# Performance work log

Hardware: AMD Instinct MI355X
Metric: run time of the kernel (lower is better)

The kernel has to match this reference:

```python
import jax, jax.numpy as jnp
import numpy as np


def setup_inputs() -> dict:
    key = jax.random.key(0)
    ks = jax.random.split(key, 5)
    B, S, D = 2, 2048, 1024
    inv = 1.0 / np.sqrt(D)
    inp = {
        "x": jax.random.normal(ks[0], (B, S, D), jnp.float32),
        "Wq": jax.random.normal(ks[1], (D, D), jnp.float32) * inv,
        "bq": jnp.zeros((D,), jnp.float32),
        "Wk": jax.random.normal(ks[2], (D, D), jnp.float32) * inv,
        "bk": jnp.zeros((D,), jnp.float32),
        "Wv": jax.random.normal(ks[3], (D, D), jnp.float32) * inv,
        "bv": jnp.zeros((D,), jnp.float32),
        "Wo": jax.random.normal(ks[4], (D, D), jnp.float32) * inv,
        "bo": jnp.zeros((D,), jnp.float32),
        "num_heads": 16,
        "window_size": 128,
    }
    return inp


def reference(x, Wq, bq, Wk, bk, Wv, bv, Wo, bo, num_heads, window_size):
    B, S, D = x.shape
    H = num_heads
    hd = D // H
    scale = 1.0 / np.sqrt(hd)

    def split_heads(t):  # [B,S,D] -> [B,H,S,hd]
        return t.reshape(B, S, H, hd).transpose(0, 2, 1, 3)

    q = split_heads(x @ Wq + bq)
    k = split_heads(x @ Wk + bk)
    v = split_heads(x @ Wv + bv)

    # dense scores, then sliding-window + causal mask (faithful to original)
    scores = jnp.einsum('bhqd,bhkd->bhqk', q, k) * scale  # [B,H,S,S]
    i = jnp.arange(S)[:, None]
    j = jnp.arange(S)[None, :]
    # position i attends to j in [i - window_size + 1, i]
    mask = (j <= i) & (j > i - window_size)
    scores = jnp.where(mask, scores, -jnp.inf)
    attn_weights = jax.nn.softmax(scores, axis=-1)  # dropout is identity in eval

    out = jnp.einsum('bhqk,bhkd->bhqd', attn_weights, v)  # [B,H,S,hd]
    out = out.transpose(0, 2, 1, 3).reshape(B, S, D)
    return out @ Wo + bo, attn_weights
```

## Files before the change

kernel.cpp:

```cpp
#include <hip/hip_runtime.h>
#include <cmath>

typedef __attribute__((ext_vector_type(8))) __bf16 v8bf;
typedef __attribute__((ext_vector_type(4))) float  v4f;

#define DEV static __device__ __forceinline__

DEV unsigned short f2bf(float f) {
  unsigned u = __builtin_bit_cast(unsigned, f);
  unsigned r = u + 0x7fffu + ((u >> 16) & 1u);
  return (unsigned short)(r >> 16);
}
DEV float bf2f(unsigned short s) {
  return __builtin_bit_cast(float, ((unsigned)s) << 16);
}
DEV v8bf ld8(const unsigned short* p) { return *(const v8bf*)p; }

DEV void gl16(const unsigned short* g, unsigned short* l) {
  __builtin_amdgcn_global_load_lds(
      (const __attribute__((address_space(1))) unsigned int*)g,
      (__attribute__((address_space(3))) unsigned int*)l, 16, 0, 0);
}

DEV void zero_rows(float* __restrict__ wout, int rbase, int wave, int lane) {
  int r0 = rbase + wave * 4;
  for (int rr = 0; rr < 4; rr++) {
    int row = r0 + rr;
    int i = row & 2047;
    int lo = i - 127;
    float* rowp = wout + (size_t)row * 2048;
#pragma unroll
    for (int it = 0; it < 8; it++) {
      int col = it * 256 + lane * 4;
      bool full_in = (col >= lo) && (col + 3 <= i);
      if (full_in) continue;
      bool overlap = (col + 3 >= lo) && (col <= i);
      if (!overlap) {
        v4f z = {0.f, 0.f, 0.f, 0.f};
        __builtin_nontemporal_store(z, (v4f*)(rowp + col));
      } else {
#pragma unroll
        for (int e = 0; e < 4; e++) {
          int j = col + e;
          if (j < lo || j > i) rowp[j] = 0.f;
        }
      }
    }
  }
}

__global__ __launch_bounds__(256) void k_prep(const float* __restrict__ x,
                                              const float* __restrict__ Wq,
                                              const float* __restrict__ Wk,
                                              const float* __restrict__ Wv,
                                              const float* __restrict__ Wo,
                                              const float* __restrict__ bq,
                                              const float* __restrict__ bk,
                                              const float* __restrict__ bv,
                                              unsigned short* __restrict__ xb,
                                              unsigned short* __restrict__ WT,
                                              unsigned short* __restrict__ WoT,
                                              float* __restrict__ bqkv) {
  __shared__ float t[32][33];
  int bx = blockIdx.x, tid = threadIdx.x;
  if (bx < 4096) {
    int i = bx * 256 + tid;
    float4 v = ((const float4*)x)[i];
    unsigned lo = (unsigned)f2bf(v.x) | ((unsigned)f2bf(v.y) << 16);
    unsigned hi = (unsigned)f2bf(v.z) | ((unsigned)f2bf(v.w) << 16);
    ((uint2*)xb)[i] = make_uint2(lo, hi);
  } else if (bx < 8192) {
    int rem = bx - 4096;
    int z = rem >> 10, r2 = rem & 1023;
    const float* src = (z == 0) ? Wq : (z == 1) ? Wk : (z == 2) ? Wv : Wo;
    unsigned short* dst = (z < 3) ? WT + z * 1048576 : WoT;
    int n0 = (r2 & 31) * 32, k0 = (r2 >> 5) * 32;
    int tx = tid & 31, ty = tid >> 5;
    for (int r = ty; r < 32; r += 8)
      t[r][tx] = src[(k0 + r) * 1024 + n0 + tx];
    __syncthreads();
    for (int r = ty; r < 32; r += 8)
      dst[(n0 + r) * 1024 + k0 + tx] = f2bf(t[tx][r]);
  } else {
    int i = (bx - 8192) * 256 + tid;
    float v = (i < 1024) ? bq[i] : (i < 2048 ? bk[i - 1024] : bv[i - 2048]);
    bqkv[i] = v;
  }
}

__global__ __launch_bounds__(256) void k_gemm1(const unsigned short* __restrict__ A,
                                               const unsigned short* __restrict__ Bt,
                                               const float* __restrict__ bias,
                                               unsigned short* __restrict__ Cout,
                                               float* __restrict__ wout) {
  constexpr int K = 1024;
  __shared__ __attribute__((aligned(16))) unsigned short As[128 * 32];
  __shared__ __attribute__((aligned(16))) unsigned short Bs[128 * 32];
  int tid = threadIdx.x;
  int wave = tid >> 6, lane = tid & 63;
  int bx = blockIdx.x;
  if (!(bx % 3 == 0 && bx < 2304)) {
    int wid = (bx < 2304) ? (bx - (bx + 2) / 3) : (1536 + bx - 2304);
    zero_rows(wout, wid * 16, wave, lane);
    return;
  }
  int gid = bx / 3;
  int n0 = (gid % 24) * 128, m0 = (gid / 24) * 128;
  int wm = (wave >> 1) * 64, wn = (wave & 1) * 64;
  int m = lane & 15, q4 = lane >> 4;
  int arow = tid >> 2, acol = (tid & 3) * 8;
  v4f acc[4][4] = {};
  const unsigned short* ga0 = A + (m0 + arow) * K + acol;
  const unsigned short* ga1 = A + (m0 + 64 + arow) * K + acol;
  const unsigned short* gb0 = Bt + (n0 + arow) * K + acol;
  const unsigned short* gb1 = Bt + (n0 + 64 + arow) * K + acol;
  unsigned short* lA0 = As + wave * 512;
  unsigned short* lA1 = As + 2048 + wave * 512;
  unsigned short* lB0 = Bs + wave * 512;
  unsigned short* lB1 = Bs + 2048 + wave * 512;

  for (int kt = 0; kt < K; kt += 32) {
    gl16(ga0 + kt, lA0);
    gl16(ga1 + kt, lA1);
    gl16(gb0 + kt, lB0);
    gl16(gb1 + kt, lB1);
    __syncthreads();
    v8bf af[4], bfv[4];
#pragma unroll
    for (int mt = 0; mt < 4; mt++) af[mt] = ld8(&As[(wm + mt * 16 + m) * 32 + q4 * 8]);
#pragma unroll
    for (int nt = 0; nt < 4; nt++) bfv[nt] = ld8(&Bs[(wn + nt * 16 + m) * 32 + q4 * 8]);
#pragma unroll
    for (int mt = 0; mt < 4; mt++)
#pragma unroll
      for (int nt = 0; nt < 4; nt++)
        acc[mt][nt] = __builtin_amdgcn_mfma_f32_16x16x32_bf16(af[mt], bfv[nt], acc[mt][nt], 0, 0, 0);
    __syncthreads();
  }
#pragma unroll
  for (int mt = 0; mt < 4; mt++)
#pragma unroll
    for (int nt = 0; nt < 4; nt++) {
      int col = n0 + wn + nt * 16 + m;
      float bb = bias[col];
#pragma unroll
      for (int r = 0; r < 4; r++) {
        int row = m0 + wm + mt * 16 + q4 * 4 + r;
        Cout[row * 3072 + col] = f2bf(acc[mt][nt][r] + bb);
      }
    }
}

__global__ __launch_bounds__(256) void k_transv(const unsigned short* __restrict__ QKV,
                                                unsigned short* __restrict__ Vtg) {
  __shared__ unsigned short t[32][33];
  int bx = blockIdx.x, tid = threadIdx.x;
  int st = bx & 63, h2 = (bx >> 6) & 1, bh = bx >> 7;
  int b = bh >> 4, h = bh & 15;
  int s0 = st * 32, d0 = h2 * 32;
  int tx = tid & 31, ty = tid >> 5;
  const unsigned short* src = QKV + (size_t)b * 2048 * 3072 + 2048 + h * 64 + d0;
  for (int r = ty; r < 32; r += 8)
    t[r][tx] = src[(size_t)(s0 + r) * 3072 + tx];
  __syncthreads();
  unsigned short* dst = Vtg + (size_t)(bh * 64 + d0) * 2048 + s0;
  for (int r = ty; r < 32; r += 8)
    dst[(size_t)r * 2048 + tx] = t[tx][r];
}

__global__ __launch_bounds__(256) void k_attn(const unsigned short* __restrict__ QKV,
                                              const unsigned short* __restrict__ Vtg,
                                              unsigned short* __restrict__ Oatt,
                                              float* __restrict__ wout) {
  constexpr int VTS = 208;
  constexpr int PSS = 168;
  __shared__ __attribute__((aligned(16))) unsigned short Vt[64 * VTS];
  __shared__ __attribute__((aligned(16))) unsigned short Ps[4][16 * PSS];
  int tid = threadIdx.x, wave = tid >> 6, lane = tid & 63;
  int bx = blockIdx.x;
  if (bx >= 32) {
    int wid = (bx - 32) + 40 * (blockIdx.y + 16 * blockIdx.z);
    zero_rows(wout, 28672 + wid * 16, wave, lane);
    return;
  }
  int b = blockIdx.z, h = blockIdx.y, i0 = bx * 64;
  int kbase = i0 - 128;
  const int ld = 3072;
  const unsigned short* Qg = QKV + b * 2048 * ld + h * 64;
  const unsigned short* Kg = Qg + 1024;

  const unsigned short* vsrc = Vtg + (size_t)(b * 16 + h) * 64 * 2048;
  for (int idx = tid; idx < 1536; idx += 256) {
    int row = idx / 24, c16 = idx % 24;
    int gcol = kbase + c16 * 8;
    if (gcol < 0) gcol = 0;
    v8bf vv = ld8(vsrc + (size_t)row * 2048 + gcol);
    *(v8bf*)&Vt[row * VTS + c16 * 8] = vv;
  }
  {
    int row = tid >> 2, c4 = (tid & 3) * 4;
    *(uint2*)&Vt[row * VTS + 192 + c4] = make_uint2(0u, 0u);
  }
  for (int c = lane; c < 16 * 24; c += 64)
    Ps[wave][(c / 24) * PSS + 144 + (c % 24)] = 0;
  __syncthreads();

  int qb = i0 + wave * 16;
  int m = lane & 15, q4 = lane >> 4;

  const unsigned short* qrow = Qg + (qb + m) * ld;
  v8bf qa0 = ld8(qrow + q4 * 8);
  v8bf qa1 = ld8(qrow + 32 + q4 * 8);

  v4f sc[9];
#pragma unroll
  for (int n = 0; n < 9; n++) {
    int key = kbase + wave * 16 + n * 16 + m;
    int kg = key < 0 ? 0 : key;
    const unsigned short* krow = Kg + kg * ld;
    v8bf kb0 = ld8(krow + q4 * 8);
    v8bf kb1 = ld8(krow + 32 + q4 * 8);
    v4f z = {0.f, 0.f, 0.f, 0.f};
    z = __builtin_amdgcn_mfma_f32_16x16x32_bf16(qa0, kb0, z, 0, 0, 0);
    z = __builtin_amdgcn_mfma_f32_16x16x32_bf16(qa1, kb1, z, 0, 0, 0);
    sc[n] = z;
  }
  float mx[4] = {-3e38f, -3e38f, -3e38f, -3e38f};
#pragma unroll
  for (int n = 0; n < 9; n++)
#pragma unroll
    for (int r = 0; r < 4; r++) {
      int i = qb + q4 * 4 + r;
      int j = kbase + wave * 16 + n * 16 + m;
      float v = sc[n][r] * 0.125f;
      bool ok = (j >= 0) && (j <= i) && (j > i - 128);
      v = ok ? v : -3e38f;
      sc[n][r] = v;
      mx[r] = fmaxf(mx[r], v);
    }
#pragma unroll
  for (int o = 1; o < 16; o <<= 1)
#pragma unroll
    for (int r = 0; r < 4; r++) mx[r] = fmaxf(mx[r], __shfl_xor(mx[r], o, 64));
  float sum[4] = {0.f, 0.f, 0.f, 0.f};
#pragma unroll
  for (int n = 0; n < 9; n++)
#pragma unroll
    for (int r = 0; r < 4; r++) {
      float p = __expf(sc[n][r] - mx[r]);
      sc[n][r] = p;
      sum[r] += p;
    }
#pragma unroll
  for (int o = 1; o < 16; o <<= 1)
#pragma unroll
    for (int r = 0; r < 4; r++) sum[r] += __shfl_xor(sum[r], o, 64);
  float inv[4];
#pragma unroll
  for (int r = 0; r < 4; r++) inv[r] = 1.0f / sum[r];

#pragma unroll
  for (int n = 0; n < 9; n++)
#pragma unroll
    for (int r = 0; r < 4; r++)
      Ps[wave][(q4 * 4 + r) * PSS + n * 16 + m] = f2bf(sc[n][r] * inv[r]);
  __syncthreads();

  v4f oacc[4] = {};
#pragma unroll
  for (int c = 0; c < 5; c++) {
    v8bf pa = ld8(&Ps[wave][m * PSS + c * 32 + q4 * 8]);
#pragma unroll
    for (int dt = 0; dt < 4; dt++) {
      v8bf vb = ld8(&Vt[(dt * 16 + m) * VTS + wave * 16 + c * 32 + q4 * 8]);
      oacc[dt] = __builtin_amdgcn_mfma_f32_16x16x32_bf16(pa, vb, oacc[dt], 0, 0, 0);
    }
  }
#pragma unroll
  for (int dt = 0; dt < 4; dt++)
#pragma unroll
    for (int r = 0; r < 4; r++)
      Oatt[(b * 2048 + qb + q4 * 4 + r) * 1024 + h * 64 + dt * 16 + m] = f2bf(oacc[dt][r]);

  for (int R = 0; R < 16; R++) {
    int iq = qb + R;
    float* rowp = wout + (size_t)((b * 16 + h) * 2048 + iq) * 2048;
    int lo = iq - 127;
    int t0 = R + 1 + lane * 2;
    float p0 = bf2f(Ps[wave][R * PSS + t0]);
    float p1 = bf2f(Ps[wave][R * PSS + t0 + 1]);
    int j0 = lo + lane * 2;
    if (j0 >= 0) rowp[j0] = p0;
    if (j0 + 1 >= 0) rowp[j0 + 1] = p1;
  }
}

__global__ __launch_bounds__(256) void k_tail(const unsigned short* __restrict__ Oat,
                                              const unsigned short* __restrict__ WoT,
                                              const float* __restrict__ bo,
                                              float* __restrict__ out,
                                              float* __restrict__ wout) {
  __shared__ __attribute__((aligned(16))) unsigned short As[128 * 32];
  __shared__ __attribute__((aligned(16))) unsigned short Bs[128 * 32];
  int tid = threadIdx.x, wave = tid >> 6, lane = tid & 63;
  int bx = blockIdx.x;

  if (bx % 5 != 0) {
    int wid = bx - (bx + 4) / 5;
    zero_rows(wout, 49152 + wid * 16, wave, lane);
    return;
  }
  constexpr int K = 1024;
  int gid = bx / 5;
  int n0 = (gid & 7) * 128, m0 = (gid >> 3) * 128;
  int wm = (wave >> 1) * 64, wn = (wave & 1) * 64;
  int m = lane & 15, q4 = lane >> 4;
  int arow = tid >> 2, acol = (tid & 3) * 8;
  v4f acc[4][4] = {};
  const unsigned short* ga0 = Oat + (m0 + arow) * K + acol;
  const unsigned short* ga1 = Oat + (m0 + 64 + arow) * K + acol;
  const unsigned short* gb0 = WoT + (n0 + arow) * K + acol;
  const unsigned short* gb1 = WoT + (n0 + 64 + arow) * K + acol;
  unsigned short* lA0 = As + wave * 512;
  unsigned short* lA1 = As + 2048 + wave * 512;
  unsigned short* lB0 = Bs + wave * 512;
  unsigned short* lB1 = Bs + 2048 + wave * 512;
  for (int kt = 0; kt < K; kt += 32) {
    gl16(ga0 + kt, lA0);
    gl16(ga1 + kt, lA1);
    gl16(gb0 + kt, lB0);
    gl16(gb1 + kt, lB1);
    __syncthreads();
    v8bf af[4], bfv[4];
#pragma unroll
    for (int mt = 0; mt < 4; mt++) af[mt] = ld8(&As[(wm + mt * 16 + m) * 32 + q4 * 8]);
#pragma unroll
    for (int nt = 0; nt < 4; nt++) bfv[nt] = ld8(&Bs[(wn + nt * 16 + m) * 32 + q4 * 8]);
#pragma unroll
    for (int mt = 0; mt < 4; mt++)
#pragma unroll
      for (int nt = 0; nt < 4; nt++)
        acc[mt][nt] = __builtin_amdgcn_mfma_f32_16x16x32_bf16(af[mt], bfv[nt], acc[mt][nt], 0, 0, 0);
    __syncthreads();
  }
#pragma unroll
  for (int mt = 0; mt < 4; mt++)
#pragma unroll
    for (int nt = 0; nt < 4; nt++) {
      int col = n0 + wn + nt * 16 + m;
      float bb = bo[col];
#pragma unroll
      for (int r = 0; r < 4; r++) {
        int row = m0 + wm + mt * 16 + q4 * 4 + r;
        out[row * 1024 + col] = acc[mt][nt][r] + bb;
      }
    }
}

extern "C" void kernel_launch(void* const* d_in, const int* in_sizes, int n_in,
                              void* d_out, int out_size, void* d_ws, size_t ws_size,
                              hipStream_t stream) {
  (void)in_sizes; (void)n_in; (void)out_size; (void)ws_size;
  const float* x  = (const float*)d_in[0];
  const float* Wq = (const float*)d_in[1];
  const float* bq = (const float*)d_in[2];
  const float* Wk = (const float*)d_in[3];
  const float* bk = (const float*)d_in[4];
  const float* Wv = (const float*)d_in[5];
  const float* bv = (const float*)d_in[6];
  const float* Wo = (const float*)d_in[7];
  const float* bo = (const float*)d_in[8];

  char* ws = (char*)d_ws;
  unsigned short* xb   = (unsigned short*)(ws);
  unsigned short* WT   = (unsigned short*)(ws + 8388608);
  unsigned short* WoT  = (unsigned short*)(ws + 14680064);
  float*          bqkv = (float*)(ws + 16777216);
  unsigned short* QKV  = (unsigned short*)(ws + 16789504);
  unsigned short* Oat  = (unsigned short*)(ws + 41955328);
  unsigned short* Vtg  = (unsigned short*)(ws + 67121152);

  float* out  = (float*)d_out;
  float* wout = out + 4194304;

  k_prep<<<8204, 256, 0, stream>>>(x, Wq, Wk, Wv, Wo, bq, bk, bv, xb, WT, WoT, bqkv);
  k_gemm1<<<2560, 256, 0, stream>>>(xb, WT, bqkv, QKV, wout);
  k_transv<<<4096, 256, 0, stream>>>(QKV, Vtg);
  k_attn<<<dim3(72, 16, 2), 256, 0, stream>>>(QKV, Vtg, Oat, wout);
  k_tail<<<1280, 256, 0, stream>>>(Oat, WoT, bo, out, wout);
}
```

Measured before the change: 653.4 us.

## Fuse V transpose into QKV GEMM epilogue and interleave weight zeroing

The QKV GEMM epilogue now writes Q and K into a compact buffer and writes V directly in transposed per-head layout, which removes the separate transpose kernel and its round trip through memory. The zero-fill of the large attention-weights output is redistributed. Each GEMM block issues non-temporal zero stores inside its K loop instead of using separate zeroing blocks, attention blocks zero extra rows after their main work, and the tail kernel takes the remainder. This lets the streaming writes overlap with compute, at the cost of extra store traffic competing with GEMM loads and an uncoalesced 8-byte strided write pattern for V.

```diff
diff --git a/kernel.cpp b/kernel.cpp
--- a/kernel.cpp
+++ b/kernel.cpp
@@ -91,20 +91,15 @@
 __global__ __launch_bounds__(256) void k_gemm1(const unsigned short* __restrict__ A,
                                                const unsigned short* __restrict__ Bt,
                                                const float* __restrict__ bias,
-                                               unsigned short* __restrict__ Cout,
+                                               unsigned short* __restrict__ QK,
+                                               unsigned short* __restrict__ Vtg,
                                                float* __restrict__ wout) {
   constexpr int K = 1024;
   __shared__ __attribute__((aligned(16))) unsigned short As[128 * 32];
   __shared__ __attribute__((aligned(16))) unsigned short Bs[128 * 32];
   int tid = threadIdx.x;
   int wave = tid >> 6, lane = tid & 63;
-  int bx = blockIdx.x;
-  if (!(bx % 3 == 0 && bx < 2304)) {
-    int wid = (bx < 2304) ? (bx - (bx + 2) / 3) : (1536 + bx - 2304);
-    zero_rows(wout, wid * 16, wave, lane);
-    return;
-  }
-  int gid = bx / 3;
+  int gid = blockIdx.x;
   int n0 = (gid % 24) * 128, m0 = (gid / 24) * 128;
   int wm = (wave >> 1) * 64, wn = (wave & 1) * 64;
   int m = lane & 15, q4 = lane >> 4;
@@ -119,11 +114,18 @@
   unsigned short* lB0 = Bs + wave * 512;
   unsigned short* lB1 = Bs + 2048 + wave * 512;
 
+  v4f zz = {0.f, 0.f, 0.f, 0.f};
+  v4f* fp = (v4f*)(wout + (size_t)gid * 65536);
+  int fb = 0;
+
   for (int kt = 0; kt < K; kt += 32) {
     gl16(ga0 + kt, lA0);
     gl16(ga1 + kt, lA1);
     gl16(gb0 + kt, lB0);
     gl16(gb1 + kt, lB1);
+    __builtin_nontemporal_store(zz, fp + fb + tid * 2);
+    __builtin_nontemporal_store(zz, fp + fb + tid * 2 + 1);
+    fb += 512;
     __syncthreads();
     v8bf af[4], bfv[4];
 #pragma unroll
@@ -137,38 +139,42 @@
         acc[mt][nt] = __builtin_amdgcn_mfma_f32_16x16x32_bf16(af[mt], bfv[nt], acc[mt][nt], 0, 0, 0);
     __syncthreads();
   }
-#pragma unroll
-  for (int mt = 0; mt < 4; mt++)
-#pragma unroll
-    for (int nt = 0; nt < 4; nt++) {
-      int col = n0 + wn + nt * 16 + m;
-      float bb = bias[col];
-#pragma unroll
-      for (int r = 0; r < 4; r++) {
-        int row = m0 + wm + mt * 16 + q4 * 4 + r;
-        Cout[row * 3072 + col] = f2bf(acc[mt][nt][r] + bb);
+  if (n0 < 2048) {
+#pragma unroll
+    for (int mt = 0; mt < 4; mt++)
+#pragma unroll
+      for (int nt = 0; nt < 4; nt++) {
+        int col = n0 + wn + nt * 16 + m;
+        float bb = bias[col];
+#pragma unroll
+        for (int r = 0; r < 4; r++) {
+          int row = m0 + wm + mt * 16 + q4 * 4 + r;
+          QK[row * 2048 + col] = f2bf(acc[mt][nt][r] + bb);
+        }
       }
-    }
-}
-
-__global__ __launch_bounds__(256) void k_transv(const unsigned short* __restrict__ QKV,
-                                                unsigned short* __restrict__ Vtg) {
-  __shared__ unsigned short t[32][33];
-  int bx = blockIdx.x, tid = threadIdx.x;
-  int st = bx & 63, h2 = (bx >> 6) & 1, bh = bx >> 7;
-  int b = bh >> 4, h = bh & 15;
-  int s0 = st * 32, d0 = h2 * 32;
-  int tx = tid & 31, ty = tid >> 5;
-  const unsigned short* src = QKV + (size_t)b * 2048 * 3072 + 2048 + h * 64 + d0;
-  for (int r = ty; r < 32; r += 8)
-    t[r][tx] = src[(size_t)(s0 + r) * 3072 + tx];
-  __syncthreads();
-  unsigned short* dst = Vtg + (size_t)(bh * 64 + d0) * 2048 + s0;
-  for (int r = ty; r < 32; r += 8)
-    dst[(size_t)r * 2048 + tx] = t[tx][r];
-}
-
-__global__ __launch_bounds__(256) void k_attn(const unsigned short* __restrict__ QKV,
+  } else {
+    int b = m0 >> 11;
+#pragma unroll
+    for (int mt = 0; mt < 4; mt++)
+#pragma unroll
+      for (int nt = 0; nt < 4; nt++) {
+        int d = n0 - 2048 + wn + nt * 16 + m;
+        int h = d >> 6, dd = d & 63;
+        float bb = bias[2048 + d];
+        int vrow = (b * 16 + h) * 64 + dd;
+        int s0 = (m0 + wm + mt * 16 + q4 * 4) & 2047;
+        unsigned short u0 = f2bf(acc[mt][nt][0] + bb);
+        unsigned short u1 = f2bf(acc[mt][nt][1] + bb);
+        unsigned short u2 = f2bf(acc[mt][nt][2] + bb);
+        unsigned short u3 = f2bf(acc[mt][nt][3] + bb);
+        unsigned lo = (unsigned)u0 | ((unsigned)u1 << 16);
+        unsigned hi = (unsigned)u2 | ((unsigned)u3 << 16);
+        *(uint2*)&Vtg[(size_t)vrow * 2048 + s0] = make_uint2(lo, hi);
+      }
+  }
+}
+
+__global__ __launch_bounds__(256) void k_attn(const unsigned short* __restrict__ QK,
                                               const unsigned short* __restrict__ Vtg,
                                               unsigned short* __restrict__ Oatt,
                                               float* __restrict__ wout) {
@@ -177,16 +183,10 @@
   __shared__ __attribute__((aligned(16))) unsigned short Vt[64 * VTS];
   __shared__ __attribute__((aligned(16))) unsigned short Ps[4][16 * PSS];
   int tid = threadIdx.x, wave = tid >> 6, lane = tid & 63;
-  int bx = blockIdx.x;
-  if (bx >= 32) {
-    int wid = (bx - 32) + 40 * (blockIdx.y + 16 * blockIdx.z);
-    zero_rows(wout, 28672 + wid * 16, wave, lane);
-    return;
-  }
-  int b = blockIdx.z, h = blockIdx.y, i0 = bx * 64;
+  int b = blockIdx.z, h = blockIdx.y, i0 = blockIdx.x * 64;
   int kbase = i0 - 128;
-  const int ld = 3072;
-  const unsigned short* Qg = QKV + b * 2048 * ld + h * 64;
+  const int ld = 2048;
+  const unsigned short* Qg = QK + (size_t)b * 2048 * ld + h * 64;
   const unsigned short* Kg = Qg + 1024;
 
   const unsigned short* vsrc = Vtg + (size_t)(b * 16 + h) * 64 * 2048;
@@ -293,6 +293,9 @@
     if (j0 >= 0) rowp[j0] = p0;
     if (j0 + 1 >= 0) rowp[j0 + 1] = p1;
   }
+
+  int flat = blockIdx.x + 32 * (blockIdx.y + 16 * blockIdx.z);
+  zero_rows(wout, 24576 + flat * 16, wave, lane);
 }
 
 __global__ __launch_bounds__(256) void k_tail(const unsigned short* __restrict__ Oat,
@@ -305,14 +308,12 @@
   int tid = threadIdx.x, wave = tid >> 6, lane = tid & 63;
   int bx = blockIdx.x;
 
-  if (bx % 5 != 0) {
-    int wid = bx - (bx + 4) / 5;
-    zero_rows(wout, 49152 + wid * 16, wave, lane);
+  if (bx >= 256) {
+    zero_rows(wout, 40960 + (bx - 256) * 16, wave, lane);
     return;
   }
   constexpr int K = 1024;
-  int gid = bx / 5;
-  int n0 = (gid & 7) * 128, m0 = (gid >> 3) * 128;
+  int n0 = (bx & 7) * 128, m0 = (bx >> 3) * 128;
   int wm = (wave >> 1) * 64, wn = (wave & 1) * 64;
   int m = lane & 15, q4 = lane >> 4;
   int arow = tid >> 2, acol = (tid & 3) * 8;
@@ -376,16 +377,15 @@
   unsigned short* WT   = (unsigned short*)(ws + 8388608);
   unsigned short* WoT  = (unsigned short*)(ws + 14680064);
   float*          bqkv = (float*)(ws + 16777216);
-  unsigned short* QKV  = (unsigned short*)(ws + 16789504);
-  unsigned short* Oat  = (unsigned short*)(ws + 41955328);
-  unsigned short* Vtg  = (unsigned short*)(ws + 67121152);
+  unsigned short* QK   = (unsigned short*)(ws + 16789504);
+  unsigned short* Oat  = (unsigned short*)(ws + 33566720);
+  unsigned short* Vtg  = (unsigned short*)(ws + 41955328);
 
   float* out  = (float*)d_out;
   float* wout = out + 4194304;
 
   k_prep<<<8204, 256, 0, stream>>>(x, Wq, Wk, Wv, Wo, bq, bk, bv, xb, WT, WoT, bqkv);
-  k_gemm1<<<2560, 256, 0, stream>>>(xb, WT, bqkv, QKV, wout);
-  k_transv<<<4096, 256, 0, stream>>>(QKV, Vtg);
-  k_attn<<<dim3(72, 16, 2), 256, 0, stream>>>(QKV, Vtg, Oat, wout);
-  k_tail<<<1280, 256, 0, stream>>>(Oat, WoT, bo, out, wout);
-}
+  k_gemm1<<<768, 256, 0, stream>>>(xb, WT, bqkv, QK, Vtg, wout);
+  k_attn<<<dim3(32, 16, 2), 256, 0, stream>>>(QK, Vtg, Oat, wout);
+  k_tail<<<1792, 256, 0, stream>>>(Oat, WoT, bo, out, wout);
+}
```

New measurement: 643.1 us. Within noise of the previous version (-1.6%).
